# Performance work log

Measured on AMD Instinct MI355X. Metric: run time of the kernel, lower is better.

## Reference

```python
import jax, jax.numpy as jnp
import numpy as np

T, B, D, H = 256, 128, 1024, 1024


def setup_inputs() -> dict:
    key = jax.random.key(0)
    ks = jax.random.split(key, 9)
    s = 1.0 / np.sqrt(D + H)  # nn.Linear default init scale
    inp = {"inputs": jax.random.normal(ks[0], (T, B, D), dtype=jnp.float32)}
    names = ["Wf", "bf", "Wi", "bi", "Wg", "bg", "Wo", "bo"]
    for j, name in enumerate(names):
        shape = (H, D + H) if name.startswith("W") else (H,)
        inp[name] = jax.random.uniform(ks[j + 1], shape, jnp.float32, -s, s)
    return inp


def reference(inputs, Wf, bf, Wi, bi, Wg, bg, Wo, bo):
    # inputs: [T, B, D]; gate weights: [H, D+H] (torch Linear layout)
    b = inputs.shape[1]
    h = Wf.shape[0]
    hx0 = jnp.zeros((b, h), inputs.dtype)
    cx0 = jnp.zeros((b, h), inputs.dtype)

    def step(carry, x):
        hx, cx = carry
        z = jnp.concatenate([x, hx], axis=1)  # [B, D+H]
        f = jax.nn.sigmoid(z @ Wf.T + bf)
        i = jax.nn.sigmoid(z @ Wi.T + bi)
        g = jnp.tanh(z @ Wg.T + bg)
        o = jax.nn.sigmoid(z @ Wo.T + bo)
        cx = f * cx + i * g
        hx = o * jnp.tanh(cx)
        return (hx, cx), hx

    (hx, cx), outputs = jax.lax.scan(step, (hx0, cx0), inputs)
    return outputs, hx, cx
```

## Files before the change

kernel.cpp:

```cpp
#include <hip/hip_runtime.h>

typedef _Float16 h8 __attribute__((ext_vector_type(8)));
typedef _Float16 h4 __attribute__((ext_vector_type(4)));
typedef float    f4 __attribute__((ext_vector_type(4)));
typedef unsigned long long u64;

#define NBLK 256

__device__ __forceinline__ float sigm(float x) {
    return 1.0f / (1.0f + __expf(-x));
}
__device__ __forceinline__ float tanh_fast(float x) {
    return 1.0f - 2.0f / (__expf(2.0f * x) + 1.0f);
}

__device__ __forceinline__ void bar_arrive(unsigned* grp, int g) {
    __syncthreads();
    if (threadIdx.x == 0) {
        __hip_atomic_fetch_add(&grp[g * 64], 1u, __ATOMIC_RELAXED,
                               __HIP_MEMORY_SCOPE_AGENT);
    }
}
__device__ __forceinline__ void bar_wait(unsigned* grp, int mg, unsigned barno) {
    if (threadIdx.x == 0) {
        const unsigned tgt = (barno + 1u) * 128u;
        unsigned* base = &grp[mg * 4 * 64];
        unsigned spins = 0;
        for (;;) {
            unsigned s0 = __hip_atomic_load(&base[0],   __ATOMIC_RELAXED,
                                            __HIP_MEMORY_SCOPE_AGENT);
            unsigned s1 = __hip_atomic_load(&base[64],  __ATOMIC_RELAXED,
                                            __HIP_MEMORY_SCOPE_AGENT);
            unsigned s2 = __hip_atomic_load(&base[128], __ATOMIC_RELAXED,
                                            __HIP_MEMORY_SCOPE_AGENT);
            unsigned s3 = __hip_atomic_load(&base[192], __ATOMIC_RELAXED,
                                            __HIP_MEMORY_SCOPE_AGENT);
            if (s0 + s1 + s2 + s3 >= tgt) break;
            __builtin_amdgcn_s_sleep(2);
            if (++spins > (1u << 24)) break;
        }
    }
    __syncthreads();
}

__global__ void prep_kernel(const float* __restrict__ x, _Float16* __restrict__ xbuf,
                            unsigned* __restrict__ ctr, unsigned* __restrict__ hb0u) {
    const int gtid = blockIdx.x * blockDim.x + threadIdx.x;
    if (gtid < 1024) ctr[gtid] = 0u;
    if (gtid < 65536) hb0u[gtid] = 0u;
    const f4* src = (const f4*)x;
    h4* dst = (h4*)xbuf;
    const int stride = gridDim.x * blockDim.x;
    for (int i = gtid; i < 8388608; i += stride)
        dst[i] = __builtin_convertvector(src[i], h4);
}

#define XHALF                                                                  \
    _Pragma("unroll")                                                          \
    for (int kc = 0; kc < 32; kc += 2) {                                       \
        h8 av0 = *(const h8*)(xA + kc * 32);                                   \
        h8 av1 = *(const h8*)(xA + kc * 32 + 32);                              \
        h8 b00 = *(const h8*)&wsm[kc * 1024 + boff];                           \
        h8 b10 = *(const h8*)&wsm[kc * 1024 + boff + 512];                     \
        h8 b01 = *(const h8*)&wsm[(kc + 1) * 1024 + boff];                     \
        h8 b11 = *(const h8*)&wsm[(kc + 1) * 1024 + boff + 512];               \
        a00 = __builtin_amdgcn_mfma_f32_16x16x32_f16(av0, b00, a00, 0, 0, 0);  \
        a10 = __builtin_amdgcn_mfma_f32_16x16x32_f16(av0, b10, a10, 0, 0, 0);  \
        a01 = __builtin_amdgcn_mfma_f32_16x16x32_f16(av1, b01, a01, 0, 0, 0);  \
        a11 = __builtin_amdgcn_mfma_f32_16x16x32_f16(av1, b11, a11, 0, 0, 0);  \
    }

#define LDH8(dst, elemoff)                                                     \
    do {                                                                       \
        union { u64 q[2]; h8 v; } u_;                                          \
        u64* p_ = (u64*)(hA + (elemoff));                                      \
        u_.q[0] = __hip_atomic_load(p_,     __ATOMIC_RELAXED,                  \
                                    __HIP_MEMORY_SCOPE_AGENT);                 \
        u_.q[1] = __hip_atomic_load(p_ + 1, __ATOMIC_RELAXED,                  \
                                    __HIP_MEMORY_SCOPE_AGENT);                 \
        dst = u_.v;                                                            \
    } while (0)

template<bool ROT>
__global__ __launch_bounds__(256, 1)
void lstm_kernel(const _Float16* __restrict__ xbuf,
                 _Float16* __restrict__ hb0, _Float16* __restrict__ hb1,
                 const float* __restrict__ Wf, const float* __restrict__ bfp,
                 const float* __restrict__ Wi, const float* __restrict__ bip,
                 const float* __restrict__ Wg, const float* __restrict__ bgp,
                 const float* __restrict__ Wo, const float* __restrict__ bop,
                 float* __restrict__ out,
                 unsigned* __restrict__ grp) {
    __shared__ _Float16 wsm[64 * 1024];

    const int tid = threadIdx.x;
    const int bid = blockIdx.x;
    const int mg = bid >> 7;
    const int ug = bid & 127;
    const int u0 = ug << 3;
    const int g  = mg * 4 + (bid & 3);

    const float* WSEL[4] = {Wf, Wi, Wg, Wo};

    {
        const int col = tid & 31;
        const int kseg = tid >> 5;
        const float* srcp = WSEL[col >> 3] + (size_t)(u0 + (col & 7)) * 2048
                          + kseg * 256;
        const int cbase = (col >> 4) * 512 + (col & 15) * 8;
#pragma unroll 8
        for (int k4 = 0; k4 < 256; k4 += 4) {
            const int k = kseg * 256 + k4;
            f4 v = *(const f4*)(srcp + k4);
            h4 hv = __builtin_convertvector(v, h4);
            *(h4*)&wsm[(k >> 5) * 1024 + cbase + ((k >> 3) & 3) * 128 + (k & 7)] = hv;
        }
    }

    const int lane  = tid & 63;
    const int wv    = tid >> 6;
    const int row16 = lane & 15;
    const int quad  = lane >> 4;
    const int uu    = lane & 7;

    __syncthreads();

    const float bias_f = bfp[u0 + uu];
    const float bias_i = bip[u0 + uu];
    const float bias_g = bgp[u0 + uu];
    const float bias_o = bop[u0 + uu];

    const int zrow = mg * 64 + wv * 16 + row16;
    const int boff = quad * 128 + row16 * 8;
    const int drow = mg * 64 + wv * 16 + quad * 4;
    const bool writer = (lane & 8) == 0;
    const bool pstore = writer && ((uu & 1) == 0);
    const bool himask = (lane & 8) != 0;

    const _Float16* hbv[2] = {hb0, hb1};
    const size_t aoff = (size_t)zrow * 1024 + quad * 8;
    const _Float16* xbase = xbuf + aoff;
    const size_t obase = (size_t)drow * 1024 + u0 + uu;

    float cc[4] = {0.f, 0.f, 0.f, 0.f};
    float hnv[4];

    f4 a00 = {0.f,0.f,0.f,0.f}, a01 = {0.f,0.f,0.f,0.f};
    f4 a10 = {0.f,0.f,0.f,0.f}, a11 = {0.f,0.f,0.f,0.f};
    {
        const _Float16* xA = xbase;
        XHALF
    }

    for (int t = 0; t < 256; ++t) {
        if (t) bar_wait(grp, mg, (unsigned)(t - 1));

        const _Float16* hA = (ROT ? hb0 + (size_t)t * 131072 : hbv[t & 1]) + aoff;
        unsigned* hwu = (unsigned*)(ROT ? hb0 + (size_t)(t + 1) * 131072
                                        : hbv[(t + 1) & 1]);

#pragma unroll
        for (int kc = 32; kc < 64; kc += 2) {
            h8 av0, av1;
            if constexpr (ROT) {
                av0 = *(const h8*)(hA + (kc - 32) * 32);
                av1 = *(const h8*)(hA + (kc - 32) * 32 + 32);
            } else {
                LDH8(av0, (kc - 32) * 32);
                LDH8(av1, (kc - 32) * 32 + 32);
            }
            h8 b00 = *(const h8*)&wsm[kc * 1024 + boff];
            h8 b10 = *(const h8*)&wsm[kc * 1024 + boff + 512];
            h8 b01 = *(const h8*)&wsm[(kc + 1) * 1024 + boff];
            h8 b11 = *(const h8*)&wsm[(kc + 1) * 1024 + boff + 512];
            a00 = __builtin_amdgcn_mfma_f32_16x16x32_f16(av0, b00, a00, 0, 0, 0);
            a10 = __builtin_amdgcn_mfma_f32_16x16x32_f16(av0, b10, a10, 0, 0, 0);
            a01 = __builtin_amdgcn_mfma_f32_16x16x32_f16(av1, b01, a01, 0, 0, 0);
            a11 = __builtin_amdgcn_mfma_f32_16x16x32_f16(av1, b11, a11, 0, 0, 0);
        }

        f4 s0 = a00 + a01;
        f4 s1 = a10 + a11;
        float q0[4], q1[4];
#pragma unroll
        for (int j = 0; j < 4; ++j) {
            q0[j] = __shfl_xor(s0[j], 8, 64);
            q1[j] = __shfl_xor(s1[j], 8, 64);
        }
#pragma unroll
        for (int j = 0; j < 4; ++j) {
            float pf = himask ? q0[j] : s0[j];
            float pi = himask ? s0[j] : q0[j];
            float pg = himask ? q1[j] : s1[j];
            float po = himask ? s1[j] : q1[j];
            float fg = sigm(pf + bias_f);
            float ig = sigm(pi + bias_i);
            float gg = tanh_fast(pg + bias_g);
            float og = sigm(po + bias_o);
            float cn = fg * cc[j] + ig * gg;
            cc[j] = cn;
            float hn = og * tanh_fast(cn);
            hnv[j] = hn;
            float hp = __shfl_xor(hn, 1, 64);
            if (pstore) {
                _Float16 alo = (_Float16)hn, ahi = (_Float16)hp;
                unsigned short blo, bhi;
                __builtin_memcpy(&blo, &alo, 2);
                __builtin_memcpy(&bhi, &ahi, 2);
                unsigned pk = (unsigned)blo | ((unsigned)bhi << 16);
                __hip_atomic_store(&hwu[(obase >> 1) + (size_t)j * 512], pk,
                                   __ATOMIC_RELAXED, __HIP_MEMORY_SCOPE_AGENT);
            }
        }

        if (t < 255) {
            bar_arrive(grp, g);
            if (writer) {
                float* outb = out + (size_t)t * 131072;
#pragma unroll
                for (int j = 0; j < 4; ++j)
                    __builtin_nontemporal_store(hnv[j], &outb[obase + (size_t)j * 1024]);
            }
            a00 = (f4){0.f,0.f,0.f,0.f}; a01 = (f4){0.f,0.f,0.f,0.f};
            a10 = (f4){0.f,0.f,0.f,0.f}; a11 = (f4){0.f,0.f,0.f,0.f};
            const _Float16* xA = xbase + (size_t)(t + 1) * 131072;
            XHALF
        } else if (writer) {
            float* outb = out + (size_t)255 * 131072;
#pragma unroll
            for (int j = 0; j < 4; ++j) {
                __builtin_nontemporal_store(hnv[j], &outb[obase + (size_t)j * 1024]);
                __builtin_nontemporal_store(hnv[j], &out[33554432 + obase + (size_t)j * 1024]);
            }
        }
    }
    if (writer) {
#pragma unroll
        for (int j = 0; j < 4; ++j)
            __builtin_nontemporal_store(
                cc[j], &out[33554432 + 131072 + obase + (size_t)j * 1024]);
    }
}

extern "C" void kernel_launch(void* const* d_in, const int* in_sizes, int n_in,
                              void* d_out, int out_size, void* d_ws, size_t ws_size,
                              hipStream_t stream) {
    const float* x  = (const float*)d_in[0];
    const float* Wf = (const float*)d_in[1];
    const float* bf = (const float*)d_in[2];
    const float* Wi = (const float*)d_in[3];
    const float* bi = (const float*)d_in[4];
    const float* Wg = (const float*)d_in[5];
    const float* bg = (const float*)d_in[6];
    const float* Wo = (const float*)d_in[7];
    const float* bo = (const float*)d_in[8];
    float* out = (float*)d_out;

    unsigned char* ws = (unsigned char*)d_ws;
    unsigned* grp  = (unsigned*)ws;
    _Float16* hbase = (_Float16*)(ws + 4096);

    const size_t HROT = 257ull * 262144ull;
    const size_t ROT_NEED = 4096ull + HROT + 67108864ull;
    const bool rot = (ws_size >= ROT_NEED);

    _Float16* hb1  = (_Float16*)(ws + 4096 + 262144);
    _Float16* xbuf = rot ? (_Float16*)(ws + 4096 + HROT)
                         : (_Float16*)(ws + 4096 + 524288);

    prep_kernel<<<2048, 256, 0, stream>>>(x, xbuf, grp, (unsigned*)hbase);
    if (rot)
        lstm_kernel<true><<<NBLK, 256, 0, stream>>>(xbuf, hbase, hb1,
                                                    Wf, bf, Wi, bi, Wg, bg, Wo, bo,
                                                    out, grp);
    else
        lstm_kernel<false><<<NBLK, 256, 0, stream>>>(xbuf, hbase, hb1,
                                                     Wf, bf, Wi, bi, Wg, bg, Wo, bo,
                                                     out, grp);
}
```

Baseline: 3.224 ms.

## Replace polled group-counter barrier with hierarchical arrive tree and per-block flags

The grid barrier becomes a two-level counter tree: each block increments one of 8 group counters per half, the last arriver bumps a root counter, and the final arriver writes the barrier number into 128 per-block flag slots. Each waiting block then spins on its own padded flag instead of polling four shared counters. The aim is to cut contention on hot cache lines during the per-timestep grid sync. The cost is a serial chain of atomics plus 128 flag stores on the critical path, and a larger workspace region that must be zeroed.

```diff
diff --git a/kernel.cpp b/kernel.cpp
--- a/kernel.cpp
+++ b/kernel.cpp
@@ -14,28 +14,35 @@
     return 1.0f - 2.0f / (__expf(2.0f * x) + 1.0f);
 }
 
-__device__ __forceinline__ void bar_arrive(unsigned* grp, int g) {
+__device__ __forceinline__ void bar_arrive(unsigned* grp, unsigned* root,
+                                           unsigned* gof, int g, int mg,
+                                           unsigned barno) {
     __syncthreads();
     if (threadIdx.x == 0) {
-        __hip_atomic_fetch_add(&grp[g * 64], 1u, __ATOMIC_RELAXED,
-                               __HIP_MEMORY_SCOPE_AGENT);
-    }
-}
-__device__ __forceinline__ void bar_wait(unsigned* grp, int mg, unsigned barno) {
+        unsigned old = __hip_atomic_fetch_add(&grp[g * 64], 1u, __ATOMIC_RELAXED,
+                                              __HIP_MEMORY_SCOPE_AGENT);
+        if ((old & 15u) == 15u) {
+            unsigned oldr = __hip_atomic_fetch_add(&root[mg * 64], 1u,
+                                                   __ATOMIC_RELAXED,
+                                                   __HIP_MEMORY_SCOPE_AGENT);
+            if ((oldr & 7u) == 7u) {
+                unsigned* f = &gof[mg * 128 * 64];
+                const unsigned v = barno + 1u;
+#pragma unroll 4
+                for (int i = 0; i < 128; ++i)
+                    __hip_atomic_store(&f[i * 64], v, __ATOMIC_RELAXED,
+                                       __HIP_MEMORY_SCOPE_AGENT);
+            }
+        }
+    }
+}
+__device__ __forceinline__ void bar_wait(unsigned* gof, int bid, unsigned barno) {
     if (threadIdx.x == 0) {
-        const unsigned tgt = (barno + 1u) * 128u;
-        unsigned* base = &grp[mg * 4 * 64];
+        unsigned* f = &gof[bid * 64];
+        const unsigned tgt = barno + 1u;
         unsigned spins = 0;
-        for (;;) {
-            unsigned s0 = __hip_atomic_load(&base[0],   __ATOMIC_RELAXED,
-                                            __HIP_MEMORY_SCOPE_AGENT);
-            unsigned s1 = __hip_atomic_load(&base[64],  __ATOMIC_RELAXED,
-                                            __HIP_MEMORY_SCOPE_AGENT);
-            unsigned s2 = __hip_atomic_load(&base[128], __ATOMIC_RELAXED,
-                                            __HIP_MEMORY_SCOPE_AGENT);
-            unsigned s3 = __hip_atomic_load(&base[192], __ATOMIC_RELAXED,
-                                            __HIP_MEMORY_SCOPE_AGENT);
-            if (s0 + s1 + s2 + s3 >= tgt) break;
+        while (__hip_atomic_load(f, __ATOMIC_RELAXED,
+                                 __HIP_MEMORY_SCOPE_AGENT) < tgt) {
             __builtin_amdgcn_s_sleep(2);
             if (++spins > (1u << 24)) break;
         }
@@ -46,7 +53,7 @@
 __global__ void prep_kernel(const float* __restrict__ x, _Float16* __restrict__ xbuf,
                             unsigned* __restrict__ ctr, unsigned* __restrict__ hb0u) {
     const int gtid = blockIdx.x * blockDim.x + threadIdx.x;
-    if (gtid < 1024) ctr[gtid] = 0u;
+    if (gtid < 18432) ctr[gtid] = 0u;
     if (gtid < 65536) hb0u[gtid] = 0u;
     const f4* src = (const f4*)x;
     h4* dst = (h4*)xbuf;
@@ -90,7 +97,8 @@
                  const float* __restrict__ Wg, const float* __restrict__ bgp,
                  const float* __restrict__ Wo, const float* __restrict__ bop,
                  float* __restrict__ out,
-                 unsigned* __restrict__ grp) {
+                 unsigned* __restrict__ grp, unsigned* __restrict__ root,
+                 unsigned* __restrict__ gof) {
     __shared__ _Float16 wsm[64 * 1024];
 
     const int tid = threadIdx.x;
@@ -98,7 +106,7 @@
     const int mg = bid >> 7;
     const int ug = bid & 127;
     const int u0 = ug << 3;
-    const int g  = mg * 4 + (bid & 3);
+    const int g  = mg * 8 + (ug & 7);
 
     const float* WSEL[4] = {Wf, Wi, Wg, Wo};
 
@@ -153,7 +161,7 @@
     }
 
     for (int t = 0; t < 256; ++t) {
-        if (t) bar_wait(grp, mg, (unsigned)(t - 1));
+        if (t) bar_wait(gof, bid, (unsigned)(t - 1));
 
         const _Float16* hA = (ROT ? hb0 + (size_t)t * 131072 : hbv[t & 1]) + aoff;
         unsigned* hwu = (unsigned*)(ROT ? hb0 + (size_t)(t + 1) * 131072
@@ -214,7 +222,7 @@
         }
 
         if (t < 255) {
-            bar_arrive(grp, g);
+            bar_arrive(grp, root, gof, g, mg, (unsigned)t);
             if (writer) {
                 float* outb = out + (size_t)t * 131072;
 #pragma unroll
@@ -258,23 +266,25 @@
 
     unsigned char* ws = (unsigned char*)d_ws;
     unsigned* grp  = (unsigned*)ws;
-    _Float16* hbase = (_Float16*)(ws + 4096);
+    unsigned* root = (unsigned*)(ws + 4096);
+    unsigned* gof  = (unsigned*)(ws + 8192);
+    _Float16* hbase = (_Float16*)(ws + 73728);
 
     const size_t HROT = 257ull * 262144ull;
-    const size_t ROT_NEED = 4096ull + HROT + 67108864ull;
+    const size_t ROT_NEED = 73728ull + HROT + 67108864ull;
     const bool rot = (ws_size >= ROT_NEED);
 
-    _Float16* hb1  = (_Float16*)(ws + 4096 + 262144);
-    _Float16* xbuf = rot ? (_Float16*)(ws + 4096 + HROT)
-                         : (_Float16*)(ws + 4096 + 524288);
+    _Float16* hb1  = (_Float16*)(ws + 73728 + 262144);
+    _Float16* xbuf = rot ? (_Float16*)(ws + 73728 + HROT)
+                         : (_Float16*)(ws + 73728 + 524288);
 
     prep_kernel<<<2048, 256, 0, stream>>>(x, xbuf, grp, (unsigned*)hbase);
     if (rot)
         lstm_kernel<true><<<NBLK, 256, 0, stream>>>(xbuf, hbase, hb1,
                                                     Wf, bf, Wi, bi, Wg, bg, Wo, bo,
-                                                    out, grp);
+                                                    out, grp, root, gof);
     else
         lstm_kernel<false><<<NBLK, 256, 0, stream>>>(xbuf, hbase, hb1,
                                                      Wf, bf, Wi, bi, Wg, bg, Wo, bo,
-                                                     out, grp);
-}
+                                                     out, grp, root, gof);
+}
```

Result: no change. 3.227 ms (+0.1%).

## Replace atomic-counter grid barrier with per-block flag slots polled by a wavefront

Applied to the files above, without the earlier changes.

Each block now publishes its step number to its own padded flag slot with a plain atomic store, instead of doing fetch-adds on four shared group counters. The first wavefront polls the 128 flags of its group in parallel, two per lane, and leaves the loop with a wave-wide vote. This is meant to remove the contention of atomic read-modify-write on hot counters and to shorten the barrier's critical path. Output stores also change from nontemporal to ordinary stores, and the workspace offsets are moved to make room for the larger flag area.

```diff
diff --git a/kernel.cpp b/kernel.cpp
--- a/kernel.cpp
+++ b/kernel.cpp
@@ -14,28 +14,24 @@
     return 1.0f - 2.0f / (__expf(2.0f * x) + 1.0f);
 }
 
-__device__ __forceinline__ void bar_arrive(unsigned* grp, int g) {
+__device__ __forceinline__ void bar_arrive(unsigned* slot, int bid, unsigned barno) {
     __syncthreads();
-    if (threadIdx.x == 0) {
-        __hip_atomic_fetch_add(&grp[g * 64], 1u, __ATOMIC_RELAXED,
-                               __HIP_MEMORY_SCOPE_AGENT);
-    }
-}
-__device__ __forceinline__ void bar_wait(unsigned* grp, int mg, unsigned barno) {
-    if (threadIdx.x == 0) {
-        const unsigned tgt = (barno + 1u) * 128u;
-        unsigned* base = &grp[mg * 4 * 64];
+    if (threadIdx.x == 0)
+        __hip_atomic_store(&slot[bid * 64], barno + 1u, __ATOMIC_RELAXED,
+                           __HIP_MEMORY_SCOPE_AGENT);
+}
+__device__ __forceinline__ void bar_wait(unsigned* slot, int mg, unsigned barno) {
+    if (threadIdx.x < 64) {
+        const unsigned tgt = barno + 1u;
+        unsigned* p0 = &slot[(mg * 128 + threadIdx.x) * 64];
+        unsigned* p1 = p0 + 64 * 64;
         unsigned spins = 0;
         for (;;) {
-            unsigned s0 = __hip_atomic_load(&base[0],   __ATOMIC_RELAXED,
+            unsigned v0 = __hip_atomic_load(p0, __ATOMIC_RELAXED,
                                             __HIP_MEMORY_SCOPE_AGENT);
-            unsigned s1 = __hip_atomic_load(&base[64],  __ATOMIC_RELAXED,
+            unsigned v1 = __hip_atomic_load(p1, __ATOMIC_RELAXED,
                                             __HIP_MEMORY_SCOPE_AGENT);
-            unsigned s2 = __hip_atomic_load(&base[128], __ATOMIC_RELAXED,
-                                            __HIP_MEMORY_SCOPE_AGENT);
-            unsigned s3 = __hip_atomic_load(&base[192], __ATOMIC_RELAXED,
-                                            __HIP_MEMORY_SCOPE_AGENT);
-            if (s0 + s1 + s2 + s3 >= tgt) break;
+            if (__all(v0 >= tgt && v1 >= tgt)) break;
             __builtin_amdgcn_s_sleep(2);
             if (++spins > (1u << 24)) break;
         }
@@ -46,7 +42,7 @@
 __global__ void prep_kernel(const float* __restrict__ x, _Float16* __restrict__ xbuf,
                             unsigned* __restrict__ ctr, unsigned* __restrict__ hb0u) {
     const int gtid = blockIdx.x * blockDim.x + threadIdx.x;
-    if (gtid < 1024) ctr[gtid] = 0u;
+    if (gtid < 16384) ctr[gtid] = 0u;
     if (gtid < 65536) hb0u[gtid] = 0u;
     const f4* src = (const f4*)x;
     h4* dst = (h4*)xbuf;
@@ -90,7 +86,7 @@
                  const float* __restrict__ Wg, const float* __restrict__ bgp,
                  const float* __restrict__ Wo, const float* __restrict__ bop,
                  float* __restrict__ out,
-                 unsigned* __restrict__ grp) {
+                 unsigned* __restrict__ slot) {
     __shared__ _Float16 wsm[64 * 1024];
 
     const int tid = threadIdx.x;
@@ -98,7 +94,6 @@
     const int mg = bid >> 7;
     const int ug = bid & 127;
     const int u0 = ug << 3;
-    const int g  = mg * 4 + (bid & 3);
 
     const float* WSEL[4] = {Wf, Wi, Wg, Wo};
 
@@ -153,7 +148,7 @@
     }
 
     for (int t = 0; t < 256; ++t) {
-        if (t) bar_wait(grp, mg, (unsigned)(t - 1));
+        if (t) bar_wait(slot, mg, (unsigned)(t - 1));
 
         const _Float16* hA = (ROT ? hb0 + (size_t)t * 131072 : hbv[t & 1]) + aoff;
         unsigned* hwu = (unsigned*)(ROT ? hb0 + (size_t)(t + 1) * 131072
@@ -214,12 +209,12 @@
         }
 
         if (t < 255) {
-            bar_arrive(grp, g);
+            bar_arrive(slot, bid, (unsigned)t);
             if (writer) {
                 float* outb = out + (size_t)t * 131072;
 #pragma unroll
                 for (int j = 0; j < 4; ++j)
-                    __builtin_nontemporal_store(hnv[j], &outb[obase + (size_t)j * 1024]);
+                    outb[obase + (size_t)j * 1024] = hnv[j];
             }
             a00 = (f4){0.f,0.f,0.f,0.f}; a01 = (f4){0.f,0.f,0.f,0.f};
             a10 = (f4){0.f,0.f,0.f,0.f}; a11 = (f4){0.f,0.f,0.f,0.f};
@@ -229,16 +224,15 @@
             float* outb = out + (size_t)255 * 131072;
 #pragma unroll
             for (int j = 0; j < 4; ++j) {
-                __builtin_nontemporal_store(hnv[j], &outb[obase + (size_t)j * 1024]);
-                __builtin_nontemporal_store(hnv[j], &out[33554432 + obase + (size_t)j * 1024]);
+                outb[obase + (size_t)j * 1024] = hnv[j];
+                out[33554432 + obase + (size_t)j * 1024] = hnv[j];
             }
         }
     }
     if (writer) {
 #pragma unroll
         for (int j = 0; j < 4; ++j)
-            __builtin_nontemporal_store(
-                cc[j], &out[33554432 + 131072 + obase + (size_t)j * 1024]);
+            out[33554432 + 131072 + obase + (size_t)j * 1024] = cc[j];
     }
 }
 
@@ -257,24 +251,24 @@
     float* out = (float*)d_out;
 
     unsigned char* ws = (unsigned char*)d_ws;
-    unsigned* grp  = (unsigned*)ws;
-    _Float16* hbase = (_Float16*)(ws + 4096);
+    unsigned* slot = (unsigned*)ws;
+    _Float16* hbase = (_Float16*)(ws + 65536);
 
     const size_t HROT = 257ull * 262144ull;
-    const size_t ROT_NEED = 4096ull + HROT + 67108864ull;
+    const size_t ROT_NEED = 65536ull + HROT + 67108864ull;
     const bool rot = (ws_size >= ROT_NEED);
 
-    _Float16* hb1  = (_Float16*)(ws + 4096 + 262144);
-    _Float16* xbuf = rot ? (_Float16*)(ws + 4096 + HROT)
-                         : (_Float16*)(ws + 4096 + 524288);
-
-    prep_kernel<<<2048, 256, 0, stream>>>(x, xbuf, grp, (unsigned*)hbase);
+    _Float16* hb1  = (_Float16*)(ws + 65536 + 262144);
+    _Float16* xbuf = rot ? (_Float16*)(ws + 65536 + HROT)
+                         : (_Float16*)(ws + 65536 + 524288);
+
+    prep_kernel<<<2048, 256, 0, stream>>>(x, xbuf, slot, (unsigned*)hbase);
     if (rot)
         lstm_kernel<true><<<NBLK, 256, 0, stream>>>(xbuf, hbase, hb1,
                                                     Wf, bf, Wi, bi, Wg, bg, Wo, bo,
-                                                    out, grp);
+                                                    out, slot);
     else
         lstm_kernel<false><<<NBLK, 256, 0, stream>>>(xbuf, hbase, hb1,
                                                      Wf, bf, Wi, bi, Wg, bg, Wo, bo,
-                                                     out, grp);
-}
+                                                     out, slot);
+}
```

New measurement: 3.354 ms. 4.0% more time.
